# Optimization experiments

Hardware: AMD Instinct MI355X
Metric: run time of the kernel (lower is better)

The kernel has to match this reference:

```python
import jax, jax.numpy as jnp
import numpy as np

N = 100000
E = 1600000
EMB = 128
OUT = 64
NEG_SLOPE = 0.2


def setup_inputs() -> dict:
    key = jax.random.key(0)
    ks = jax.random.split(key, 16)
    def lin(k, fan_in, fan_out):
        bound = 1.0 / np.sqrt(fan_in)
        kw, kb = jax.random.split(k)
        w = jax.random.uniform(kw, (fan_in, fan_out), jnp.float32, -bound, bound)
        b = jax.random.uniform(kb, (fan_out,), jnp.float32, -bound, bound)
        return w, b
    x = jax.random.normal(ks[0], (N, 2 + EMB), jnp.float32)
    edge_index = jax.random.randint(ks[1], (2, E), 0, N, jnp.int64)
    w1, b1 = lin(ks[2], 1, OUT)
    w2, b2 = lin(ks[3], 1, OUT)
    gat_w = jax.random.normal(ks[4], (EMB, OUT), jnp.float32) * (1.0 / np.sqrt(EMB))
    gat_asrc = jax.random.normal(ks[5], (OUT,), jnp.float32) * (1.0 / np.sqrt(OUT))
    gat_adst = jax.random.normal(ks[6], (OUT,), jnp.float32) * (1.0 / np.sqrt(OUT))
    gat_b = jnp.zeros((OUT,), jnp.float32)
    fc1_w, fc1_b = lin(ks[7], 3 * OUT, 3 * 128)
    fc2_w, fc2_b = lin(ks[8], 3 * 128, 128)
    fc3_w, fc3_b = lin(ks[9], 128, OUT)
    return {"x": x, "edge_index": edge_index,
            "w1": w1, "b1": b1, "w2": w2, "b2": b2,
            "gat_w": gat_w, "gat_asrc": gat_asrc, "gat_adst": gat_adst, "gat_b": gat_b,
            "fc1_w": fc1_w, "fc1_b": fc1_b, "fc2_w": fc2_w, "fc2_b": fc2_b,
            "fc3_w": fc3_w, "fc3_b": fc3_b}


def _gat(x3, edge_index, w, a_src, a_dst, bias):
    n = x3.shape[0]
    h = x3 @ w  # [N, OUT]
    # add self-loops (PyG GATConv default)
    loops = jnp.arange(n, dtype=edge_index.dtype)
    src = jnp.concatenate([edge_index[0], loops])
    dst = jnp.concatenate([edge_index[1], loops])
    alpha_s = h @ a_src  # [N]
    alpha_d = h @ a_dst  # [N]
    e = jax.nn.leaky_relu(alpha_s[src] + alpha_d[dst], NEG_SLOPE)  # [E+N]
    # softmax over incoming edges per destination node
    m = jax.ops.segment_max(e, dst, num_segments=n)
    m = jnp.where(jnp.isfinite(m), m, 0.0)
    ex = jnp.exp(e - m[dst])
    denom = jax.ops.segment_sum(ex, dst, num_segments=n)
    alpha = ex / (denom[dst] + 1e-16)
    out = jax.ops.segment_sum(alpha[:, None] * h[src], dst, num_segments=n)
    return out + bias


def reference(x, edge_index, w1, b1, w2, b2, gat_w, gat_asrc, gat_adst, gat_b,
              fc1_w, fc1_b, fc2_w, fc2_b, fc3_w, fc3_b):
    x1 = x[:, 0:1] @ w1 + b1          # [N, OUT]
    x2 = x[:, 1:2] @ w2 + b2          # [N, OUT]
    x3 = _gat(x[:, 2:], edge_index, gat_w, gat_asrc, gat_adst, gat_b)  # [N, OUT]
    h = jnp.concatenate([x1, x2, x3], axis=1)  # [N, 3*OUT]
    h = jax.nn.relu(h @ fc1_w + fc1_b)
    h = jax.nn.relu(h @ fc2_w + fc2_b)
    return h @ fc3_w + fc3_b
```

## Files before the change

### kernel.cpp

```cpp
#include <hip/hip_runtime.h>
#include <math.h>

#define NSLOPE 0.2f
#define BIN_CH 8192
#define P2_CAP 5120
#define BKT_CAP 5120

typedef __attribute__((ext_vector_type(8)))  short bf16x8;
typedef __attribute__((ext_vector_type(4)))  float floatx4;
typedef __attribute__((ext_vector_type(16))) float floatx16;
typedef __attribute__((ext_vector_type(2)))  unsigned uswap2;

__device__ __forceinline__ unsigned short f2bf(float f) {
    unsigned u = __builtin_bit_cast(unsigned, f);
    u += 0x7fff + ((u >> 16) & 1);
    return (unsigned short)(u >> 16);
}
__device__ __forceinline__ float bf2f(unsigned short h) {
    unsigned u = (unsigned)h << 16;
    return __builtin_bit_cast(float, u);
}

__device__ __forceinline__ void split8(const float* v, bf16x8& hi, bf16x8& lo) {
#pragma unroll
    for (int j = 0; j < 8; j++) {
        unsigned short h = f2bf(v[j]);
        hi[j] = (short)h;
        lo[j] = (short)f2bf(v[j] - bf2f(h));
    }
}

__device__ __forceinline__ unsigned cvtpk(float a, float b) {
    unsigned r;
    asm("v_cvt_pk_bf16_f32 %0, %1, %2" : "=v"(r) : "v"(a), "v"(b));
    return r;
}

__device__ __forceinline__ uswap2 pl32swap(unsigned a, unsigned b) {
    return __builtin_amdgcn_permlane32_swap(a, b, false, false);
}

__device__ __forceinline__ bf16x8 mk8(unsigned w0, unsigned w1, unsigned w2, unsigned w3) {
    union { unsigned u[4]; bf16x8 v; } t;
    t.u[0] = w0; t.u[1] = w1; t.u[2] = w2; t.u[3] = w3;
    return t.v;
}

__device__ __forceinline__ void pack_swap(const float* v, bf16x8& f0, bf16x8& f1) {
    unsigned p00 = cvtpk(v[0],  v[1]);
    unsigned p01 = cvtpk(v[2],  v[3]);
    unsigned p10 = cvtpk(v[4],  v[5]);
    unsigned p11 = cvtpk(v[6],  v[7]);
    unsigned p20 = cvtpk(v[8],  v[9]);
    unsigned p21 = cvtpk(v[10], v[11]);
    unsigned p30 = cvtpk(v[12], v[13]);
    unsigned p31 = cvtpk(v[14], v[15]);
    uswap2 s00 = pl32swap(p00, p10);
    uswap2 s01 = pl32swap(p01, p11);
    uswap2 s10 = pl32swap(p20, p30);
    uswap2 s11 = pl32swap(p21, p31);
    f0 = mk8(s00[0], s01[0], s00[1], s01[1]);
    f1 = mk8(s10[0], s11[0], s10[1], s11[1]);
}

__global__ __launch_bounds__(256, 2)
void hproj_kernel(const float* __restrict__ x,
                  const unsigned short* __restrict__ Bhi,
                  const unsigned short* __restrict__ Blo,
                  const float* __restrict__ asrc, const float* __restrict__ adst,
                  unsigned short* __restrict__ hb, float* __restrict__ alS,
                  float* __restrict__ alD, int M)
{
    const int lane = threadIdx.x & 63;
    const int wv   = threadIdx.x >> 6;
    const int l15  = lane & 15;
    const int quad = lane >> 4;
    const int m0   = blockIdx.x * 128 + wv * 32;
    const int lane8 = lane * 8;

    floatx4 acc[2][4];
#pragma unroll
    for (int mt = 0; mt < 2; mt++)
#pragma unroll
        for (int nt = 0; nt < 4; nt++) acc[mt][nt] = (floatx4){0.f, 0.f, 0.f, 0.f};

    int r0 = m0 + l15;      if (r0 >= M) r0 = M - 1;
    int r1 = m0 + 16 + l15; if (r1 >= M) r1 = M - 1;
    const float* a0 = x + (size_t)r0 * 130 + 2 + quad * 8;
    const float* a1 = x + (size_t)r1 * 130 + 2 + quad * 8;

#pragma unroll
    for (int kt = 0; kt < 4; kt++) {
        const int kb = kt * 32;
        float av[2][8];
#pragma unroll
        for (int j = 0; j < 4; j++) {
            float2 q0 = *(const float2*)(a0 + kb + 2 * j);
            float2 q1 = *(const float2*)(a1 + kb + 2 * j);
            av[0][2 * j] = q0.x; av[0][2 * j + 1] = q0.y;
            av[1][2 * j] = q1.x; av[1][2 * j + 1] = q1.y;
        }
        bf16x8 ah[2], al[2];
        split8(av[0], ah[0], al[0]);
        split8(av[1], ah[1], al[1]);
#pragma unroll
        for (int nt = 0; nt < 4; nt++) {
            const size_t boff = (size_t)(nt * 4 + kt) * 512 + lane8;
            bf16x8 bh = *(const bf16x8*)(Bhi + boff);
            bf16x8 bl = *(const bf16x8*)(Blo + boff);
#pragma unroll
            for (int mt = 0; mt < 2; mt++) {
                acc[mt][nt] = __builtin_amdgcn_mfma_f32_16x16x32_bf16(ah[mt], bh, acc[mt][nt], 0, 0, 0);
                acc[mt][nt] = __builtin_amdgcn_mfma_f32_16x16x32_bf16(ah[mt], bl, acc[mt][nt], 0, 0, 0);
                acc[mt][nt] = __builtin_amdgcn_mfma_f32_16x16x32_bf16(al[mt], bh, acc[mt][nt], 0, 0, 0);
            }
        }
    }

    float as4[4], ad4[4];
#pragma unroll
    for (int nt = 0; nt < 4; nt++) {
        as4[nt] = asrc[nt * 16 + l15];
        ad4[nt] = adst[nt * 16 + l15];
    }

    float ps[2][4], pd[2][4];
#pragma unroll
    for (int mt = 0; mt < 2; mt++) {
#pragma unroll
        for (int r = 0; r < 4; r++) {
            int row = m0 + mt * 16 + quad * 4 + r;
            float s = 0.f, d = 0.f;
#pragma unroll
            for (int nt = 0; nt < 4; nt++) {
                float v = acc[mt][nt][r];
                s += v * as4[nt];
                d += v * ad4[nt];
                if (row < M) hb[(size_t)row * 64 + nt * 16 + l15] = f2bf(v);
            }
            ps[mt][r] = s; pd[mt][r] = d;
        }
    }
#pragma unroll
    for (int mt = 0; mt < 2; mt++)
#pragma unroll
        for (int r = 0; r < 4; r++) {
#pragma unroll
            for (int msk = 1; msk < 16; msk <<= 1) {
                ps[mt][r] += __shfl_xor(ps[mt][r], msk);
                pd[mt][r] += __shfl_xor(pd[mt][r], msk);
            }
        }
    if (l15 == 0) {
#pragma unroll
        for (int mt = 0; mt < 2; mt++)
#pragma unroll
            for (int r = 0; r < 4; r++) {
                int row = m0 + mt * 16 + quad * 4 + r;
                if (row < M) { alS[row] = ps[mt][r]; alD[row] = pd[mt][r]; }
            }
    }
}

__global__ __launch_bounds__(128, 2)
void fused_mlp(const float* __restrict__ x3,
               const float* __restrict__ x,
               const unsigned short* __restrict__ f1Hi,
               const unsigned short* __restrict__ f2Hi,
               const unsigned short* __restrict__ f3Hi,
               const unsigned short* __restrict__ f3Lo,
               const float* __restrict__ cb, const float* __restrict__ u1,
               const float* __restrict__ u2, const float* __restrict__ fc2b,
               const float* __restrict__ fc3b,
               float* __restrict__ out, int M)
{
    const int lane = threadIdx.x & 63;
    const int wv   = threadIdx.x >> 6;
    const int l31  = lane & 31;
    const int half = lane >> 5;
    const int m0   = blockIdx.x * 64 + wv * 32;
    const int lane8 = lane * 8;

    bf16x8 ah[4], al[4];
    int r0 = m0 + l31; if (r0 >= M) r0 = M - 1;
    {
        const float* a0 = x3 + (size_t)r0 * 64 + half * 8;
#pragma unroll
        for (int kt = 0; kt < 4; kt++) {
            float av[8];
            float4 qa = *(const float4*)(a0 + kt * 16);
            float4 qb = *(const float4*)(a0 + kt * 16 + 4);
            av[0]=qa.x; av[1]=qa.y; av[2]=qa.z; av[3]=qa.w;
            av[4]=qb.x; av[5]=qb.y; av[6]=qb.z; av[7]=qb.w;
            split8(av, ah[kt], al[kt]);
        }
    }

    float2 xv = *(const float2*)(x + (size_t)r0 * 130);

    floatx16 acc2[4];
#pragma unroll
    for (int nt = 0; nt < 4; nt++) acc2[nt] = (floatx16)(0.f);

#pragma unroll
    for (int nt = 0; nt < 12; nt++) {
        const unsigned short* wp = f1Hi + (size_t)nt * 2048 + lane8;
        bf16x8 wh[4];
#pragma unroll
        for (int kt = 0; kt < 4; kt++) wh[kt] = *(const bf16x8*)(wp + kt * 512);
        const unsigned short* w2p = f2Hi + (size_t)nt * 1024 + lane8;
        bf16x8 w2[8];
#pragma unroll
        for (int nt2 = 0; nt2 < 4; nt2++) {
            w2[2 * nt2]     = *(const bf16x8*)(w2p + nt2 * 12288);
            w2[2 * nt2 + 1] = *(const bf16x8*)(w2p + nt2 * 12288 + 512);
        }

        floatx16 acc = (floatx16)(0.f);
#pragma unroll
        for (int kt = 0; kt < 4; kt++) {
            acc = __builtin_amdgcn_mfma_f32_32x32x16_bf16(wh[kt], ah[kt], acc, 0, 0, 0);
            acc = __builtin_amdgcn_mfma_f32_32x32x16_bf16(wh[kt], al[kt], acc, 0, 0, 0);
        }
        float v[16];
#pragma unroll
        for (int q = 0; q < 4; q++) {
            const int c0 = nt * 32 + q * 8 + 4 * half;
            float4 cb4 = *(const float4*)(cb + c0);
            float4 u14 = *(const float4*)(u1 + c0);
            float4 u24 = *(const float4*)(u2 + c0);
            float t0 = acc[4*q+0] + cb4.x + xv.x * u14.x + xv.y * u24.x;
            float t1 = acc[4*q+1] + cb4.y + xv.x * u14.y + xv.y * u24.y;
            float t2 = acc[4*q+2] + cb4.z + xv.x * u14.z + xv.y * u24.z;
            float t3 = acc[4*q+3] + cb4.w + xv.x * u14.w + xv.y * u24.w;
            v[4*q+0] = t0 > 0.f ? t0 : 0.f;
            v[4*q+1] = t1 > 0.f ? t1 : 0.f;
            v[4*q+2] = t2 > 0.f ? t2 : 0.f;
            v[4*q+3] = t3 > 0.f ? t3 : 0.f;
        }
        bf16x8 a2_0, a2_1;
        pack_swap(v, a2_0, a2_1);
#pragma unroll
        for (int nt2 = 0; nt2 < 4; nt2++) {
            acc2[nt2] = __builtin_amdgcn_mfma_f32_32x32x16_bf16(w2[2 * nt2],     a2_0, acc2[nt2], 0, 0, 0);
            acc2[nt2] = __builtin_amdgcn_mfma_f32_32x32x16_bf16(w2[2 * nt2 + 1], a2_1, acc2[nt2], 0, 0, 0);
        }
    }

    floatx16 acc3[2];
    acc3[0] = (floatx16)(0.f);
    acc3[1] = (floatx16)(0.f);
#pragma unroll
    for (int nt2 = 0; nt2 < 4; nt2++) {
        const unsigned short* w3p = f3Hi + (size_t)nt2 * 1024 + lane8;
        const unsigned short* w3q = f3Lo + (size_t)nt2 * 1024 + lane8;
        bf16x8 wh0 = *(const bf16x8*)(w3p);
        bf16x8 wl0 = *(const bf16x8*)(w3q);
        bf16x8 wh1 = *(const bf16x8*)(w3p + 512);
        bf16x8 wl1 = *(const bf16x8*)(w3q + 512);
        bf16x8 wh2 = *(const bf16x8*)(w3p + 4096);
        bf16x8 wl2 = *(const bf16x8*)(w3q + 4096);
        bf16x8 wh3 = *(const bf16x8*)(w3p + 4096 + 512);
        bf16x8 wl3 = *(const bf16x8*)(w3q + 4096 + 512);

        float v[16];
#pragma unroll
        for (int q = 0; q < 4; q++) {
            const int c0 = nt2 * 32 + q * 8 + 4 * half;
            float4 b4 = *(const float4*)(fc2b + c0);
            float t0 = acc2[nt2][4*q+0] + b4.x;
            float t1 = acc2[nt2][4*q+1] + b4.y;
            float t2 = acc2[nt2][4*q+2] + b4.z;
            float t3 = acc2[nt2][4*q+3] + b4.w;
            v[4*q+0] = t0 > 0.f ? t0 : 0.f;
            v[4*q+1] = t1 > 0.f ? t1 : 0.f;
            v[4*q+2] = t2 > 0.f ? t2 : 0.f;
            v[4*q+3] = t3 > 0.f ? t3 : 0.f;
        }
        bf16x8 a3_0, a3_1;
        pack_swap(v, a3_0, a3_1);
        acc3[0] = __builtin_amdgcn_mfma_f32_32x32x16_bf16(wh0, a3_0, acc3[0], 0, 0, 0);
        acc3[0] = __builtin_amdgcn_mfma_f32_32x32x16_bf16(wl0, a3_0, acc3[0], 0, 0, 0);
        acc3[0] = __builtin_amdgcn_mfma_f32_32x32x16_bf16(wh1, a3_1, acc3[0], 0, 0, 0);
        acc3[0] = __builtin_amdgcn_mfma_f32_32x32x16_bf16(wl1, a3_1, acc3[0], 0, 0, 0);
        acc3[1] = __builtin_amdgcn_mfma_f32_32x32x16_bf16(wh2, a3_0, acc3[1], 0, 0, 0);
        acc3[1] = __builtin_amdgcn_mfma_f32_32x32x16_bf16(wl2, a3_0, acc3[1], 0, 0, 0);
        acc3[1] = __builtin_amdgcn_mfma_f32_32x32x16_bf16(wh3, a3_1, acc3[1], 0, 0, 0);
        acc3[1] = __builtin_amdgcn_mfma_f32_32x32x16_bf16(wl3, a3_1, acc3[1], 0, 0, 0);
    }

    int row = m0 + l31;
    if (row < M) {
        float* op = out + (size_t)row * 64;
#pragma unroll
        for (int nt3 = 0; nt3 < 2; nt3++)
#pragma unroll
            for (int q = 0; q < 4; q++) {
                const int c0 = nt3 * 32 + q * 8 + 4 * half;
                float4 b4 = *(const float4*)(fc3b + c0);
                float4 o;
                o.x = acc3[nt3][4*q+0] + b4.x;
                o.y = acc3[nt3][4*q+1] + b4.y;
                o.z = acc3[nt3][4*q+2] + b4.z;
                o.w = acc3[nt3][4*q+3] + b4.w;
                *(float4*)(op + c0) = o;
            }
    }
}

__global__ __launch_bounds__(256)
void pack_all(const float* __restrict__ gat_w, const float* __restrict__ fc1w,
              const float* __restrict__ fc2w, const float* __restrict__ fc3w,
              unsigned short* __restrict__ gatHi, unsigned short* __restrict__ gatLo,
              unsigned short* __restrict__ f1Hi, unsigned short* __restrict__ f1Lo,
              unsigned short* __restrict__ f2Hi, unsigned short* __restrict__ f2Lo,
              unsigned short* __restrict__ f3Hi, unsigned short* __restrict__ f3Lo)
{
    int g = blockIdx.x * 256 + threadIdx.x;
    const float* W; unsigned short *hi, *lo;
    int idx, K, ldw, mode;
    if (g < 8192)        { idx = g;         W = gat_w;              hi = gatHi; lo = gatLo; K = 128; ldw = 64;  mode = 1; }
    else if (g < 32768)  { idx = g - 8192;  W = fc1w + 128 * 384;   hi = f1Hi;  lo = f1Lo;  K = 64;  ldw = 384; mode = 0; }
    else if (g < 81920)  { idx = g - 32768; W = fc2w;               hi = f2Hi;  lo = f2Lo;  K = 384; ldw = 128; mode = 0; }
    else if (g < 90112)  { idx = g - 81920; W = fc3w;               hi = f3Hi;  lo = f3Lo;  K = 128; ldw = 64;  mode = 0; }
    else return;
    int n = idx / K, k = idx - n * K;
    float v = W[(size_t)k * ldw + n];
    unsigned short h = f2bf(v);
    unsigned short l = f2bf(v - bf2f(h));
    size_t pos;
    if (mode == 0) {
        int lane = ((k >> 3) & 1) * 32 + (n & 31);
        int tile = (n >> 5) * (K >> 4) + (k >> 4);
        pos = ((size_t)tile * 64 + lane) * 8 + (k & 7);
    } else {
        int lane = ((k >> 3) & 3) * 16 + (n & 15);
        int tile = (n >> 4) * (K >> 5) + (k >> 5);
        pos = ((size_t)tile * 64 + lane) * 8 + (k & 7);
    }
    hi[pos] = h;
    lo[pos] = l;
}

__global__ void prep_u(const float* __restrict__ w1, const float* __restrict__ b1,
                       const float* __restrict__ w2, const float* __restrict__ b2,
                       const float* __restrict__ fc1w, const float* __restrict__ fc1b,
                       float* __restrict__ u1, float* __restrict__ u2, float* __restrict__ cb)
{
    int j = threadIdx.x + blockIdx.x * blockDim.x;
    if (j >= 384) return;
    float s1 = 0.f, s2 = 0.f, c = fc1b[j];
    for (int k = 0; k < 64; k++) {
        float wv = fc1w[k * 384 + j];
        s1 += w1[k] * wv; c += b1[k] * wv;
    }
    for (int k = 0; k < 64; k++) {
        float wv = fc1w[(64 + k) * 384 + j];
        s2 += w2[k] * wv; c += b2[k] * wv;
    }
    u1[j] = s1; u2[j] = s2; cb[j] = c;
}

__global__ void seed_gcur(int* __restrict__ gcur)
{
    int i = blockIdx.x * 256 + threadIdx.x;
    if (i < 512) gcur[i] = i * BKT_CAP;
}

__global__ __launch_bounds__(256)
void bin_kernel(const int* __restrict__ ei, int E, int total,
                int* __restrict__ gcur, unsigned* __restrict__ items)
{
    __shared__ unsigned       stage[BIN_CH];
    __shared__ unsigned short bidx[BIN_CH];
    __shared__ int hist[512], lofs[512], base[512], cnt2[512];
    __shared__ int pairs[256];

    const int t     = threadIdx.x;
    const int base0 = blockIdx.x * BIN_CH;
    const int cnt   = min(BIN_CH, total - base0);

    for (int b = t; b < 512; b += 256) { hist[b] = 0; cnt2[b] = 0; }
    __syncthreads();

    for (int i = t; i < cnt; i += 256) {
        int tt = base0 + i;
        int d = (tt < E) ? ei[E + tt] : (tt - E);
        atomicAdd(&hist[d >> 8], 1);
    }
    __syncthreads();

    int h0 = hist[2 * t], h1 = hist[2 * t + 1];
    pairs[t] = h0 + h1;
    __syncthreads();
    for (int off = 1; off < 256; off <<= 1) {
        int x = (t >= off) ? pairs[t - off] : 0;
        __syncthreads();
        pairs[t] += x;
        __syncthreads();
    }
    int excl = (t > 0) ? pairs[t - 1] : 0;
    lofs[2 * t]     = excl;
    lofs[2 * t + 1] = excl + h0;
    for (int b = t; b < 512; b += 256)
        if (hist[b] > 0) base[b] = atomicAdd(&gcur[b], hist[b]);
    __syncthreads();

    for (int i = t; i < cnt; i += 256) {
        int tt = base0 + i;
        int d, s;
        if (tt < E) { d = ei[E + tt]; s = ei[tt]; }
        else        { d = tt - E;     s = d;      }
        int b = d >> 8;
        int r = atomicAdd(&cnt2[b], 1);
        int p = lofs[b] + r;
        stage[p] = ((unsigned)s << 8) | (unsigned)(d & 255);
        bidx[p]  = (unsigned short)b;
    }
    __syncthreads();

    for (int j = t; j < cnt; j += 256) {
        int b = bidx[j];
        items[base[b] + (j - lofs[b])] = stage[j];
    }
}

__global__ __launch_bounds__(256)
void bucket_scan(const int* __restrict__ gcur, int* __restrict__ bucketBase)
{
    __shared__ int pairs[256];
    int t = threadIdx.x;
    int h0 = gcur[2 * t]     - (2 * t) * BKT_CAP;
    int h1 = gcur[2 * t + 1] - (2 * t + 1) * BKT_CAP;
    pairs[t] = h0 + h1;
    __syncthreads();
    for (int off = 1; off < 256; off <<= 1) {
        int x = (t >= off) ? pairs[t - off] : 0;
        __syncthreads();
        pairs[t] += x;
        __syncthreads();
    }
    int excl = (t > 0) ? pairs[t - 1] : 0;
    bucketBase[2 * t]     = excl;
    bucketBase[2 * t + 1] = excl + h0;
    if (t == 255) bucketBase[512] = pairs[255];
}

__global__ __launch_bounds__(256)
void bucket_scatter(const unsigned* __restrict__ items,
                    const int* __restrict__ bucketBase,
                    int* __restrict__ rowptr,
                    const float* __restrict__ alS, const float* __restrict__ alD,
                    uint2* __restrict__ sev, int N, int total)
{
    __shared__ int   lhist[256];
    __shared__ int   sh[256];
    __shared__ int   lcur[256];
    __shared__ uint2 buf[P2_CAP];

    const int b  = blockIdx.x;
    const int t  = threadIdx.x;
    const int n0 = b << 8;
    const int i0 = bucketBase[b];
    const int cnt = bucketBase[b + 1] - i0;
    const size_t ib = (size_t)b * BKT_CAP;

    lhist[t] = 0;
    __syncthreads();
    for (int j = t; j < cnt; j += 256)
        atomicAdd(&lhist[items[ib + j] & 255u], 1);
    __syncthreads();
    sh[t] = lhist[t];
    __syncthreads();
    for (int off = 1; off < 256; off <<= 1) {
        int x = (t >= off) ? sh[t - off] : 0;
        __syncthreads();
        sh[t] += x;
        __syncthreads();
    }
    int excl = (t > 0) ? sh[t - 1] : 0;
    if (n0 + t < N) rowptr[n0 + t] = i0 + excl;
    lcur[t] = excl;
    __syncthreads();

    const bool direct = (cnt > P2_CAP);
    for (int j = t; j < cnt; j += 256) {
        unsigned raw = items[ib + j];
        int dl = (int)(raw & 255u);
        int s  = (int)(raw >> 8);
        float v = alS[s] + alD[n0 + dl];
        v = v > 0.f ? v : NSLOPE * v;
        float ex = expf(v);
        int r = atomicAdd(&lcur[dl], 1);
        uint2 it = make_uint2((unsigned)s, __builtin_bit_cast(unsigned, ex));
        if (direct) sev[i0 + r] = it;
        else        buf[r] = it;
    }
    __syncthreads();
    if (!direct)
        for (int j = t; j < cnt; j += 256) sev[i0 + j] = buf[j];
}

__global__ __launch_bounds__(256)
void aggregate_kernel(const int* __restrict__ rowptr,
                      const uint2* __restrict__ sev,
                      const unsigned int* __restrict__ hb32,
                      const float* __restrict__ gatb,
                      float* __restrict__ x3, int N, int total)
{
    int node = blockIdx.x * 8 + (threadIdx.x >> 5);
    int l    = threadIdx.x & 31;
    int hsel = threadIdx.x & 32;
    if (node >= N) return;
    int start = rowptr[node];
    int end   = (node + 1 < N) ? rowptr[node + 1] : total;
    float ax = 0.f, ay = 0.f, den = 0.f;
    for (int p = start; p < end; p += 32) {
        int idx = p + l;
        uint2 se = (idx < end) ? sev[idx] : make_uint2(0u, 0u);
        int si = (int)se.x;
        float ex = __builtin_bit_cast(float, se.y);
        int cnt = end - p; if (cnt > 32) cnt = 32;
        int j = 0;
        for (; j + 4 <= cnt; j += 4) {
            int   s0 = __shfl(si, hsel | j),       s1 = __shfl(si, hsel | (j + 1));
            int   s2 = __shfl(si, hsel | (j + 2)), s3 = __shfl(si, hsel | (j + 3));
            float e0 = __shfl(ex, hsel | j),       e1 = __shfl(ex, hsel | (j + 1));
            float e2 = __shfl(ex, hsel | (j + 2)), e3 = __shfl(ex, hsel | (j + 3));
            unsigned w0 = hb32[(size_t)s0 * 32 + l];
            unsigned w1 = hb32[(size_t)s1 * 32 + l];
            unsigned w2 = hb32[(size_t)s2 * 32 + l];
            unsigned w3 = hb32[(size_t)s3 * 32 + l];
            den += (e0 + e1) + (e2 + e3);
            ax += e0 * bf2f((unsigned short)(w0 & 0xFFFFu));
            ay += e0 * bf2f((unsigned short)(w0 >> 16));
            ax += e1 * bf2f((unsigned short)(w1 & 0xFFFFu));
            ay += e1 * bf2f((unsigned short)(w1 >> 16));
            ax += e2 * bf2f((unsigned short)(w2 & 0xFFFFu));
            ay += e2 * bf2f((unsigned short)(w2 >> 16));
            ax += e3 * bf2f((unsigned short)(w3 & 0xFFFFu));
            ay += e3 * bf2f((unsigned short)(w3 >> 16));
        }
        for (; j < cnt; j++) {
            int   sj = __shfl(si, hsel | j);
            float ej = __shfl(ex, hsel | j);
            unsigned w = hb32[(size_t)sj * 32 + l];
            den += ej;
            ax += ej * bf2f((unsigned short)(w & 0xFFFFu));
            ay += ej * bf2f((unsigned short)(w >> 16));
        }
    }
    float inv = 1.f / (den + 1e-16f);
    float2 o;
    o.x = ax * inv + gatb[2 * l];
    o.y = ay * inv + gatb[2 * l + 1];
    *(float2*)&x3[(size_t)node * 64 + 2 * l] = o;
}

extern "C" void kernel_launch(void* const* d_in, const int* in_sizes, int n_in,
                              void* d_out, int out_size, void* d_ws, size_t ws_size,
                              hipStream_t stream)
{
    const float* x      = (const float*)d_in[0];
    const int*   ei     = (const int*)d_in[1];
    const float* w1     = (const float*)d_in[2];
    const float* b1     = (const float*)d_in[3];
    const float* w2     = (const float*)d_in[4];
    const float* b2     = (const float*)d_in[5];
    const float* gat_w  = (const float*)d_in[6];
    const float* gat_as = (const float*)d_in[7];
    const float* gat_ad = (const float*)d_in[8];
    const float* gat_b  = (const float*)d_in[9];
    const float* fc1w   = (const float*)d_in[10];
    const float* fc1b   = (const float*)d_in[11];
    const float* fc2w   = (const float*)d_in[12];
    const float* fc2b   = (const float*)d_in[13];
    const float* fc3w   = (const float*)d_in[14];
    const float* fc3b   = (const float*)d_in[15];

    const int N = in_sizes[0] / 130;
    const int E = in_sizes[1] / 2;
    const int total = E + N;
    float* out = (float*)d_out;

    float* ws = (float*)d_ws;
    size_t off = 0;
    unsigned short* hb = (unsigned short*)(ws + off); off += (size_t)N * 32;
    float* x3     = ws + off; off += (size_t)N * 64;
    float* alS    = ws + off; off += (size_t)N;
    float* alD    = ws + off; off += (size_t)N;
    float* u1     = ws + off; off += 512;
    float* u2     = ws + off; off += 512;
    float* cb     = ws + off; off += 512;
    int*   rowptr = (int*)(ws + off); off += (size_t)N;
    int*   bucketBase = (int*)(ws + off); off += 520;
    int*   gcur       = (int*)(ws + off); off += 512;
    uint2* sev    = (uint2*)(ws + off); off += (size_t)total * 2;
    unsigned* items = (unsigned*)(ws + off); off += (size_t)512 * BKT_CAP;
    unsigned short* gatHi = (unsigned short*)(ws + off); off += 4096;
    unsigned short* gatLo = (unsigned short*)(ws + off); off += 4096;
    unsigned short* f1Hi  = (unsigned short*)(ws + off); off += 12288;
    unsigned short* f1Lo  = (unsigned short*)(ws + off); off += 12288;
    unsigned short* f2Hi  = (unsigned short*)(ws + off); off += 24576;
    unsigned short* f2Lo  = (unsigned short*)(ws + off); off += 24576;
    unsigned short* f3Hi  = (unsigned short*)(ws + off); off += 4096;
    unsigned short* f3Lo  = (unsigned short*)(ws + off); off += 4096;

    prep_u<<<3, 128, 0, stream>>>(w1, b1, w2, b2, fc1w, fc1b, u1, u2, cb);
    pack_all<<<(90112 + 255) / 256, 256, 0, stream>>>(gat_w, fc1w, fc2w, fc3w,
                                                      gatHi, gatLo, f1Hi, f1Lo,
                                                      f2Hi, f2Lo, f3Hi, f3Lo);
    seed_gcur<<<2, 256, 0, stream>>>(gcur);

    hproj_kernel<<<(N + 127) / 128, 256, 0, stream>>>(x, gatHi, gatLo,
                                                      gat_as, gat_ad, hb, alS, alD, N);

    int nbin = (total + BIN_CH - 1) / BIN_CH;
    bin_kernel<<<nbin, 256, 0, stream>>>(ei, E, total, gcur, items);
    bucket_scan<<<1, 256, 0, stream>>>(gcur, bucketBase);
    int nbkt = (N + 255) / 256;
    bucket_scatter<<<nbkt, 256, 0, stream>>>(items, bucketBase, rowptr,
                                             alS, alD, sev, N, total);

    aggregate_kernel<<<(N + 7) / 8, 256, 0, stream>>>(rowptr, sev,
                                                      (const unsigned int*)hb,
                                                      gat_b, x3, N, total);

    fused_mlp<<<(N + 63) / 64, 128, 0, stream>>>(x3, x,
                                                 f1Hi, f2Hi, f3Hi, f3Lo,
                                                 cb, u1, u2, fc2b, fc3b, out, N);
}
```

Measured before the change: 292.1 us.

## Merge prep kernels, fold bucket scan into scatter, use 32x32 MFMA projection

Merges the three small setup kernels (weight packing, u-vector precompute, gcur seeding) into one launch. The single-block bucket_scan kernel is removed and each bucket_scatter block redundantly recomputes the 512-entry prefix scan in shared memory. The GAT projection is rewritten to use 32x32x16 MFMA with one row per lane. This gives vectorized bf16 stores of h and needs only a single cross-half shuffle for the attention dot products. Fewer launches and less shuffle work are traded for a redundant scan in every scatter block.

```diff
diff --git a/kernel.cpp b/kernel.cpp
--- a/kernel.cpp
+++ b/kernel.cpp
@@ -65,101 +65,73 @@
 
 __global__ __launch_bounds__(256, 2)
 void hproj_kernel(const float* __restrict__ x,
-                  const unsigned short* __restrict__ Bhi,
-                  const unsigned short* __restrict__ Blo,
+                  const unsigned short* __restrict__ Whi,
+                  const unsigned short* __restrict__ Wlo,
                   const float* __restrict__ asrc, const float* __restrict__ adst,
                   unsigned short* __restrict__ hb, float* __restrict__ alS,
                   float* __restrict__ alD, int M)
 {
     const int lane = threadIdx.x & 63;
     const int wv   = threadIdx.x >> 6;
-    const int l15  = lane & 15;
-    const int quad = lane >> 4;
+    const int l31  = lane & 31;
+    const int half = lane >> 5;
     const int m0   = blockIdx.x * 128 + wv * 32;
     const int lane8 = lane * 8;
 
-    floatx4 acc[2][4];
-#pragma unroll
-    for (int mt = 0; mt < 2; mt++)
-#pragma unroll
-        for (int nt = 0; nt < 4; nt++) acc[mt][nt] = (floatx4){0.f, 0.f, 0.f, 0.f};
-
-    int r0 = m0 + l15;      if (r0 >= M) r0 = M - 1;
-    int r1 = m0 + 16 + l15; if (r1 >= M) r1 = M - 1;
-    const float* a0 = x + (size_t)r0 * 130 + 2 + quad * 8;
-    const float* a1 = x + (size_t)r1 * 130 + 2 + quad * 8;
-
-#pragma unroll
-    for (int kt = 0; kt < 4; kt++) {
-        const int kb = kt * 32;
-        float av[2][8];
+    int r0 = m0 + l31;
+    const bool valid = (r0 < M);
+    if (!valid) r0 = M - 1;
+
+    const float* a0 = x + (size_t)r0 * 130 + 2 + half * 8;
+
+    floatx16 acc[2];
+    acc[0] = (floatx16)(0.f);
+    acc[1] = (floatx16)(0.f);
+
+#pragma unroll
+    for (int kt = 0; kt < 8; kt++) {
+        float av[8];
 #pragma unroll
         for (int j = 0; j < 4; j++) {
-            float2 q0 = *(const float2*)(a0 + kb + 2 * j);
-            float2 q1 = *(const float2*)(a1 + kb + 2 * j);
-            av[0][2 * j] = q0.x; av[0][2 * j + 1] = q0.y;
-            av[1][2 * j] = q1.x; av[1][2 * j + 1] = q1.y;
-        }
-        bf16x8 ah[2], al[2];
-        split8(av[0], ah[0], al[0]);
-        split8(av[1], ah[1], al[1]);
-#pragma unroll
-        for (int nt = 0; nt < 4; nt++) {
-            const size_t boff = (size_t)(nt * 4 + kt) * 512 + lane8;
-            bf16x8 bh = *(const bf16x8*)(Bhi + boff);
-            bf16x8 bl = *(const bf16x8*)(Blo + boff);
-#pragma unroll
-            for (int mt = 0; mt < 2; mt++) {
-                acc[mt][nt] = __builtin_amdgcn_mfma_f32_16x16x32_bf16(ah[mt], bh, acc[mt][nt], 0, 0, 0);
-                acc[mt][nt] = __builtin_amdgcn_mfma_f32_16x16x32_bf16(ah[mt], bl, acc[mt][nt], 0, 0, 0);
-                acc[mt][nt] = __builtin_amdgcn_mfma_f32_16x16x32_bf16(al[mt], bh, acc[mt][nt], 0, 0, 0);
+            float2 q = *(const float2*)(a0 + kt * 16 + 2 * j);
+            av[2 * j] = q.x; av[2 * j + 1] = q.y;
+        }
+        bf16x8 xh, xl;
+        split8(av, xh, xl);
+#pragma unroll
+        for (int nt = 0; nt < 2; nt++) {
+            const size_t w0 = (size_t)(nt * 8 + kt) * 512 + lane8;
+            bf16x8 wh = *(const bf16x8*)(Whi + w0);
+            bf16x8 wl = *(const bf16x8*)(Wlo + w0);
+            acc[nt] = __builtin_amdgcn_mfma_f32_32x32x16_bf16(wh, xh, acc[nt], 0, 0, 0);
+            acc[nt] = __builtin_amdgcn_mfma_f32_32x32x16_bf16(wl, xh, acc[nt], 0, 0, 0);
+            acc[nt] = __builtin_amdgcn_mfma_f32_32x32x16_bf16(wh, xl, acc[nt], 0, 0, 0);
+        }
+    }
+
+    float ps = 0.f, pd = 0.f;
+    unsigned short* hp = hb + (size_t)r0 * 64;
+#pragma unroll
+    for (int nt = 0; nt < 2; nt++)
+#pragma unroll
+        for (int q = 0; q < 4; q++) {
+            const int c0 = nt * 32 + q * 8 + 4 * half;
+            float4 as4 = *(const float4*)(asrc + c0);
+            float4 ad4 = *(const float4*)(adst + c0);
+            float v0 = acc[nt][4*q+0], v1 = acc[nt][4*q+1];
+            float v2 = acc[nt][4*q+2], v3 = acc[nt][4*q+3];
+            ps += v0 * as4.x + v1 * as4.y + v2 * as4.z + v3 * as4.w;
+            pd += v0 * ad4.x + v1 * ad4.y + v2 * ad4.z + v3 * ad4.w;
+            if (valid) {
+                uint2 pk;
+                pk.x = cvtpk(v0, v1);
+                pk.y = cvtpk(v2, v3);
+                *(uint2*)(hp + c0) = pk;
             }
         }
-    }
-
-    float as4[4], ad4[4];
-#pragma unroll
-    for (int nt = 0; nt < 4; nt++) {
-        as4[nt] = asrc[nt * 16 + l15];
-        ad4[nt] = adst[nt * 16 + l15];
-    }
-
-    float ps[2][4], pd[2][4];
-#pragma unroll
-    for (int mt = 0; mt < 2; mt++) {
-#pragma unroll
-        for (int r = 0; r < 4; r++) {
-            int row = m0 + mt * 16 + quad * 4 + r;
-            float s = 0.f, d = 0.f;
-#pragma unroll
-            for (int nt = 0; nt < 4; nt++) {
-                float v = acc[mt][nt][r];
-                s += v * as4[nt];
-                d += v * ad4[nt];
-                if (row < M) hb[(size_t)row * 64 + nt * 16 + l15] = f2bf(v);
-            }
-            ps[mt][r] = s; pd[mt][r] = d;
-        }
-    }
-#pragma unroll
-    for (int mt = 0; mt < 2; mt++)
-#pragma unroll
-        for (int r = 0; r < 4; r++) {
-#pragma unroll
-            for (int msk = 1; msk < 16; msk <<= 1) {
-                ps[mt][r] += __shfl_xor(ps[mt][r], msk);
-                pd[mt][r] += __shfl_xor(pd[mt][r], msk);
-            }
-        }
-    if (l15 == 0) {
-#pragma unroll
-        for (int mt = 0; mt < 2; mt++)
-#pragma unroll
-            for (int r = 0; r < 4; r++) {
-                int row = m0 + mt * 16 + quad * 4 + r;
-                if (row < M) { alS[row] = ps[mt][r]; alD[row] = pd[mt][r]; }
-            }
-    }
+    ps += __shfl_xor(ps, 32);
+    pd += __shfl_xor(pd, 32);
+    if (valid && half == 0) { alS[r0] = ps; alD[r0] = pd; }
 }
 
 __global__ __launch_bounds__(128, 2)
@@ -309,62 +281,51 @@
 }
 
 __global__ __launch_bounds__(256)
-void pack_all(const float* __restrict__ gat_w, const float* __restrict__ fc1w,
+void prep_all(const float* __restrict__ gat_w, const float* __restrict__ fc1w,
               const float* __restrict__ fc2w, const float* __restrict__ fc3w,
+              const float* __restrict__ w1, const float* __restrict__ b1,
+              const float* __restrict__ w2, const float* __restrict__ b2,
+              const float* __restrict__ fc1b,
               unsigned short* __restrict__ gatHi, unsigned short* __restrict__ gatLo,
               unsigned short* __restrict__ f1Hi, unsigned short* __restrict__ f1Lo,
               unsigned short* __restrict__ f2Hi, unsigned short* __restrict__ f2Lo,
-              unsigned short* __restrict__ f3Hi, unsigned short* __restrict__ f3Lo)
+              unsigned short* __restrict__ f3Hi, unsigned short* __restrict__ f3Lo,
+              float* __restrict__ u1, float* __restrict__ u2, float* __restrict__ cb,
+              int* __restrict__ gcur)
 {
     int g = blockIdx.x * 256 + threadIdx.x;
-    const float* W; unsigned short *hi, *lo;
-    int idx, K, ldw, mode;
-    if (g < 8192)        { idx = g;         W = gat_w;              hi = gatHi; lo = gatLo; K = 128; ldw = 64;  mode = 1; }
-    else if (g < 32768)  { idx = g - 8192;  W = fc1w + 128 * 384;   hi = f1Hi;  lo = f1Lo;  K = 64;  ldw = 384; mode = 0; }
-    else if (g < 81920)  { idx = g - 32768; W = fc2w;               hi = f2Hi;  lo = f2Lo;  K = 384; ldw = 128; mode = 0; }
-    else if (g < 90112)  { idx = g - 81920; W = fc3w;               hi = f3Hi;  lo = f3Lo;  K = 128; ldw = 64;  mode = 0; }
-    else return;
-    int n = idx / K, k = idx - n * K;
-    float v = W[(size_t)k * ldw + n];
-    unsigned short h = f2bf(v);
-    unsigned short l = f2bf(v - bf2f(h));
-    size_t pos;
-    if (mode == 0) {
+    if (g < 90112) {
+        const float* W; unsigned short *hi, *lo;
+        int idx, K, ldw;
+        if (g < 8192)       { idx = g;         W = gat_w;            hi = gatHi; lo = gatLo; K = 128; ldw = 64;  }
+        else if (g < 32768) { idx = g - 8192;  W = fc1w + 128 * 384; hi = f1Hi;  lo = f1Lo;  K = 64;  ldw = 384; }
+        else if (g < 81920) { idx = g - 32768; W = fc2w;             hi = f2Hi;  lo = f2Lo;  K = 384; ldw = 128; }
+        else                { idx = g - 81920; W = fc3w;             hi = f3Hi;  lo = f3Lo;  K = 128; ldw = 64;  }
+        int n = idx / K, k = idx - n * K;
+        float v = W[(size_t)k * ldw + n];
+        unsigned short h = f2bf(v);
+        unsigned short l = f2bf(v - bf2f(h));
         int lane = ((k >> 3) & 1) * 32 + (n & 31);
         int tile = (n >> 5) * (K >> 4) + (k >> 4);
-        pos = ((size_t)tile * 64 + lane) * 8 + (k & 7);
-    } else {
-        int lane = ((k >> 3) & 3) * 16 + (n & 15);
-        int tile = (n >> 4) * (K >> 5) + (k >> 5);
-        pos = ((size_t)tile * 64 + lane) * 8 + (k & 7);
-    }
-    hi[pos] = h;
-    lo[pos] = l;
-}
-
-__global__ void prep_u(const float* __restrict__ w1, const float* __restrict__ b1,
-                       const float* __restrict__ w2, const float* __restrict__ b2,
-                       const float* __restrict__ fc1w, const float* __restrict__ fc1b,
-                       float* __restrict__ u1, float* __restrict__ u2, float* __restrict__ cb)
-{
-    int j = threadIdx.x + blockIdx.x * blockDim.x;
-    if (j >= 384) return;
-    float s1 = 0.f, s2 = 0.f, c = fc1b[j];
-    for (int k = 0; k < 64; k++) {
-        float wv = fc1w[k * 384 + j];
-        s1 += w1[k] * wv; c += b1[k] * wv;
-    }
-    for (int k = 0; k < 64; k++) {
-        float wv = fc1w[(64 + k) * 384 + j];
-        s2 += w2[k] * wv; c += b2[k] * wv;
-    }
-    u1[j] = s1; u2[j] = s2; cb[j] = c;
-}
-
-__global__ void seed_gcur(int* __restrict__ gcur)
-{
-    int i = blockIdx.x * 256 + threadIdx.x;
-    if (i < 512) gcur[i] = i * BKT_CAP;
+        size_t pos = ((size_t)tile * 64 + lane) * 8 + (k & 7);
+        hi[pos] = h;
+        lo[pos] = l;
+    } else if (g < 90496) {
+        int j = g - 90112;
+        float s1 = 0.f, s2 = 0.f, c = fc1b[j];
+        for (int k = 0; k < 64; k++) {
+            float wv = fc1w[k * 384 + j];
+            s1 += w1[k] * wv; c += b1[k] * wv;
+        }
+        for (int k = 0; k < 64; k++) {
+            float wv = fc1w[(64 + k) * 384 + j];
+            s2 += w2[k] * wv; c += b2[k] * wv;
+        }
+        u1[j] = s1; u2[j] = s2; cb[j] = c;
+    } else if (g < 91008) {
+        int b = g - 90496;
+        gcur[b] = b * BKT_CAP;
+    }
 }
 
 __global__ __launch_bounds__(256)
@@ -426,29 +387,8 @@
 }
 
 __global__ __launch_bounds__(256)
-void bucket_scan(const int* __restrict__ gcur, int* __restrict__ bucketBase)
-{
-    __shared__ int pairs[256];
-    int t = threadIdx.x;
-    int h0 = gcur[2 * t]     - (2 * t) * BKT_CAP;
-    int h1 = gcur[2 * t + 1] - (2 * t + 1) * BKT_CAP;
-    pairs[t] = h0 + h1;
-    __syncthreads();
-    for (int off = 1; off < 256; off <<= 1) {
-        int x = (t >= off) ? pairs[t - off] : 0;
-        __syncthreads();
-        pairs[t] += x;
-        __syncthreads();
-    }
-    int excl = (t > 0) ? pairs[t - 1] : 0;
-    bucketBase[2 * t]     = excl;
-    bucketBase[2 * t + 1] = excl + h0;
-    if (t == 255) bucketBase[512] = pairs[255];
-}
-
-__global__ __launch_bounds__(256)
 void bucket_scatter(const unsigned* __restrict__ items,
-                    const int* __restrict__ bucketBase,
+                    const int* __restrict__ gcur,
                     int* __restrict__ rowptr,
                     const float* __restrict__ alS, const float* __restrict__ alD,
                     uint2* __restrict__ sev, int N, int total)
@@ -456,14 +396,32 @@
     __shared__ int   lhist[256];
     __shared__ int   sh[256];
     __shared__ int   lcur[256];
+    __shared__ int   lofs[512];
     __shared__ uint2 buf[P2_CAP];
 
     const int b  = blockIdx.x;
     const int t  = threadIdx.x;
     const int n0 = b << 8;
-    const int i0 = bucketBase[b];
-    const int cnt = bucketBase[b + 1] - i0;
     const size_t ib = (size_t)b * BKT_CAP;
+
+    {
+        int g0 = gcur[2 * t]     - (2 * t) * BKT_CAP;
+        int g1 = gcur[2 * t + 1] - (2 * t + 1) * BKT_CAP;
+        sh[t] = g0 + g1;
+        __syncthreads();
+        for (int off = 1; off < 256; off <<= 1) {
+            int x = (t >= off) ? sh[t - off] : 0;
+            __syncthreads();
+            sh[t] += x;
+            __syncthreads();
+        }
+        int excl = (t > 0) ? sh[t - 1] : 0;
+        lofs[2 * t]     = excl;
+        lofs[2 * t + 1] = excl + g0;
+        __syncthreads();
+    }
+    const int i0  = lofs[b];
+    const int cnt = gcur[b] - b * BKT_CAP;
 
     lhist[t] = 0;
     __syncthreads();
@@ -593,12 +551,11 @@
     float* u2     = ws + off; off += 512;
     float* cb     = ws + off; off += 512;
     int*   rowptr = (int*)(ws + off); off += (size_t)N;
-    int*   bucketBase = (int*)(ws + off); off += 520;
-    int*   gcur       = (int*)(ws + off); off += 512;
+    int*   gcur   = (int*)(ws + off); off += 512;
     uint2* sev    = (uint2*)(ws + off); off += (size_t)total * 2;
     unsigned* items = (unsigned*)(ws + off); off += (size_t)512 * BKT_CAP;
-    unsigned short* gatHi = (unsigned short*)(ws + off); off += 4096;
-    unsigned short* gatLo = (unsigned short*)(ws + off); off += 4096;
+    unsigned short* gatHi = (unsigned short*)(ws + off); off += 8192;
+    unsigned short* gatLo = (unsigned short*)(ws + off); off += 8192;
     unsigned short* f1Hi  = (unsigned short*)(ws + off); off += 12288;
     unsigned short* f1Lo  = (unsigned short*)(ws + off); off += 12288;
     unsigned short* f2Hi  = (unsigned short*)(ws + off); off += 24576;
@@ -606,20 +563,19 @@
     unsigned short* f3Hi  = (unsigned short*)(ws + off); off += 4096;
     unsigned short* f3Lo  = (unsigned short*)(ws + off); off += 4096;
 
-    prep_u<<<3, 128, 0, stream>>>(w1, b1, w2, b2, fc1w, fc1b, u1, u2, cb);
-    pack_all<<<(90112 + 255) / 256, 256, 0, stream>>>(gat_w, fc1w, fc2w, fc3w,
+    prep_all<<<(91008 + 255) / 256, 256, 0, stream>>>(gat_w, fc1w, fc2w, fc3w,
+                                                      w1, b1, w2, b2, fc1b,
                                                       gatHi, gatLo, f1Hi, f1Lo,
-                                                      f2Hi, f2Lo, f3Hi, f3Lo);
-    seed_gcur<<<2, 256, 0, stream>>>(gcur);
+                                                      f2Hi, f2Lo, f3Hi, f3Lo,
+                                                      u1, u2, cb, gcur);
 
     hproj_kernel<<<(N + 127) / 128, 256, 0, stream>>>(x, gatHi, gatLo,
                                                       gat_as, gat_ad, hb, alS, alD, N);
 
     int nbin = (total + BIN_CH - 1) / BIN_CH;
     bin_kernel<<<nbin, 256, 0, stream>>>(ei, E, total, gcur, items);
-    bucket_scan<<<1, 256, 0, stream>>>(gcur, bucketBase);
     int nbkt = (N + 255) / 256;
-    bucket_scatter<<<nbkt, 256, 0, stream>>>(items, bucketBase, rowptr,
+    bucket_scatter<<<nbkt, 256, 0, stream>>>(items, gcur, rowptr,
                                              alS, alD, sev, N, total);
 
     aggregate_kernel<<<(N + 7) / 8, 256, 0, stream>>>(rowptr, sev,
```

After: 290.4 us. About the same (-0.6%).
